# Kernel tuning notes

Measured on AMD Instinct MI355X. Metric: run time of the kernel, lower is better.

Reference implementation:

```python
import jax, jax.numpy as jnp
import numpy as np

B, T, C, H = 4, 2048, 1024, 16
D = C // H


def setup_inputs() -> dict:
    key = jax.random.key(0)
    ks = jax.random.split(key, 6)
    s = 1.0 / np.sqrt(C)
    return {
        "x": jax.random.normal(ks[0], (B, T, C), dtype=jnp.float32),
        "attention_mask": jnp.ones((B, 1, T), dtype=jnp.int32),
        "Wq": jax.random.normal(ks[1], (C, C), dtype=jnp.float32) * s,
        "bq": jnp.zeros((C,), dtype=jnp.float32),
        "Wk": jax.random.normal(ks[2], (C, C), dtype=jnp.float32) * s,
        "bk": jnp.zeros((C,), dtype=jnp.float32),
        "Wv": jax.random.normal(ks[3], (C, C), dtype=jnp.float32) * s,
        "bv": jnp.zeros((C,), dtype=jnp.float32),
        "Wp": jax.random.normal(ks[4], (C, C), dtype=jnp.float32) * s,
        "bp": jnp.zeros((C,), dtype=jnp.float32),
    }


def reference(x, attention_mask, Wq, bq, Wk, bk, Wv, bv, Wp, bp):
    b, t, c = x.shape
    d = c // H
    # projections (torch Linear: x @ W^T + b)
    q = (x @ Wq.T + bq).reshape(b, t, H, d).transpose(0, 2, 1, 3)  # [B,H,T,D]
    k = (x @ Wk.T + bk).reshape(b, t, H, d).transpose(0, 2, 1, 3)
    v = (x @ Wv.T + bv).reshape(b, t, H, d).transpose(0, 2, 1, 3)
    attn = jnp.einsum("bhqd,bhkd->bhqk", q, k) / jnp.sqrt(jnp.asarray(d, x.dtype))
    mask = attention_mask[:, :, :t]  # [B,1,T] -> broadcast over [B,H,T,T] keys
    attn = jnp.where(mask[:, :, None, :] == 0, jnp.asarray(-jnp.inf, x.dtype), attn)
    attn = jax.nn.softmax(attn, axis=-1)  # dropout p=0 (eval)
    y = jnp.einsum("bhqk,bhkd->bhqd", attn, v)
    y = y.transpose(0, 2, 1, 3).reshape(b, t, c)
    return y @ Wp.T + bp
```

## Files before the change

kernel.cpp:

```cpp
#include <hip/hip_runtime.h>


#define TT 2048
#define CC 1024
#define HH 16
#define DD 64
#define BB 4

typedef unsigned short u16;
typedef unsigned int u32;
typedef __attribute__((ext_vector_type(8))) short bf16x8;
typedef __attribute__((ext_vector_type(4))) float f32x4;
typedef __attribute__((ext_vector_type(4))) u32 u32x4;

#if __has_builtin(__builtin_amdgcn_exp2f)
#define EXP2(x) __builtin_amdgcn_exp2f(x)
#else
#define EXP2(x) __expf((x) * 0.6931471805599453f)
#endif

__device__ __forceinline__ u16 f2bf(float f) {
    u32 u = __builtin_bit_cast(u32, f);
    u += 0x7FFFu + ((u >> 16) & 1u);
    return (u16)(u >> 16);
}
__device__ __forceinline__ u32 pk2(float a, float b) {
    u32 ua = __builtin_bit_cast(u32, a); ua += 0x7FFFu + ((ua >> 16) & 1u);
    u32 ub = __builtin_bit_cast(u32, b); ub += 0x7FFFu + ((ub >> 16) & 1u);
    return __builtin_amdgcn_perm(ub, ua, 0x07060302);
}
__device__ __forceinline__ u32 cvtpk(float lo, float hi) {
    u32 r;
    asm("v_cvt_pk_bf16_f32 %0, %1, %2" : "=v"(r) : "v"(lo), "v"(hi));
    return r;
}

#define GLDS(g, l) __builtin_amdgcn_global_load_lds( \
    (const __attribute__((address_space(1))) void*)(g), \
    (__attribute__((address_space(3))) void*)(l), 16, 0, 0)

__global__ __launch_bounds__(256) void wcvt(const float* __restrict__ s,
                                            u16* __restrict__ d, int n8) {
    const int i = blockIdx.x * 256 + threadIdx.x;
    if (i < n8) {
        const float4 f0 = ((const float4*)s)[2 * i];
        const float4 f1 = ((const float4*)s)[2 * i + 1];
        uint4 w;
        w.x = pk2(f0.x, f0.y); w.y = pk2(f0.z, f0.w);
        w.z = pk2(f1.x, f1.y); w.w = pk2(f1.z, f1.w);
        ((uint4*)d)[i] = w;
    }
}

__global__ __launch_bounds__(256) void wcvtA(const float* __restrict__ x,
                                             const float* __restrict__ Wq,
                                             const float* __restrict__ Wk,
                                             const float* __restrict__ Wv,
                                             u16* __restrict__ xb,
                                             u16* __restrict__ Wq16,
                                             u16* __restrict__ Wk16,
                                             u16* __restrict__ Wv16) {
    const int bid = blockIdx.x;
    const float* s; u16* d; int i;
    if (bid < 4096) {
        s = x; d = xb; i = bid * 256 + threadIdx.x;
    } else {
        const int t = bid - 4096;
        const int which = t >> 9, sub = t & 511;
        s = (which == 0) ? Wq : (which == 1) ? Wk : Wv;
        d = (which == 0) ? Wq16 : (which == 1) ? Wk16 : Wv16;
        i = sub * 256 + threadIdx.x;
    }
    const float4 f0 = ((const float4*)s)[2 * i];
    const float4 f1 = ((const float4*)s)[2 * i + 1];
    uint4 w;
    w.x = pk2(f0.x, f0.y); w.y = pk2(f0.z, f0.w);
    w.z = pk2(f1.x, f1.y); w.w = pk2(f1.z, f1.w);
    ((uint4*)d)[i] = w;
}

template <int BN, int WM, int WN, int MODE>
__global__ __launch_bounds__(512, 4) void gemmT(const u16* __restrict__ Ag,
                                                const u16* __restrict__ Bg,
                                                const float* __restrict__ b0,
                                                const float* __restrict__ b1,
                                                const float* __restrict__ b2,
                                                u16* __restrict__ outQ,
                                                u16* __restrict__ outK,
                                                u16* __restrict__ outV,
                                                float* __restrict__ outF) {
    constexpr int NI = WM / 16, NJ = WN / 16;
    constexpr int WAVES_N = BN / WN;
    constexpr int BUFSZ = (256 + BN) * 32;
    constexpr int SPT = 2 + BN / 128;
    constexpr int NT = CC / 32;

    extern __shared__ u16 lds[];
    const int tid  = threadIdx.x;
    const int wave = tid >> 6, lane = tid & 63;
    const int quad = lane >> 4, l16 = lane & 15;
    const int wr = wave / WAVES_N, wc = wave & (WAVES_N - 1);

    constexpr int NBX = (MODE == 0 ? 3072 : 1024) / BN;
    const int bid0 = blockIdx.y * NBX + blockIdx.x;
    const int chunk = (NBX * 32) >> 3;
    const int bid  = (bid0 & 7) * chunk + (bid0 >> 3);
    const int bn = (bid % NBX) * BN, bm = (bid / NBX) * 256;

    u32 aOff[2]; int aDst[2];
#pragma unroll
    for (int g = 0; g < 2; g++) {
        const int c = g * 512 + tid;
        const int row = c >> 2;
        const int kc = (c & 3) ^ ((row >> 1) & 3);
        aOff[g] = (u32)(bm + row) * CC + kc * 8;
        aDst[g] = c * 8;
    }
    u32 bOff[BN / 128]; int bDst[BN / 128];
#pragma unroll
    for (int g = 0; g < BN / 128; g++) {
        const int c = g * 512 + tid;
        const int row = c >> 2;
        const int kc = (c & 3) ^ ((row >> 1) & 3);
        bOff[g] = (u32)(bn + row) * CC + kc * 8;
        bDst[g] = 8192 + c * 8;
    }

    int aRd[NI], bRd[NJ];
#pragma unroll
    for (int i = 0; i < NI; i++) {
        const int row = wr * WM + i * 16 + l16;
        const int p = quad ^ ((row >> 1) & 3);
        aRd[i] = row * 32 + p * 8;
    }
#pragma unroll
    for (int j = 0; j < NJ; j++) {
        const int row = wc * WN + j * 16 + l16;
        const int p = quad ^ ((row >> 1) & 3);
        bRd[j] = 8192 + row * 32 + p * 8;
    }

    f32x4 acc[NI][NJ] = {};

#define STAGE_T(t)                                                        \
    {                                                                     \
        u16* dst = &lds[((t) % 3) * BUFSZ];                               \
        const int k0 = (t) * 32;                                          \
        _Pragma("unroll")                                                 \
        for (int g = 0; g < 2; g++)                                       \
            GLDS(&Ag[(size_t)aOff[g] + k0], &dst[aDst[g]]);               \
        _Pragma("unroll")                                                 \
        for (int g = 0; g < BN / 128; g++)                                \
            GLDS(&Bg[(size_t)bOff[g] + k0], &dst[bDst[g]]);               \
    }

#define COMPUTE_T(t)                                                      \
    {                                                                     \
        const u16* buf = &lds[((t) % 3) * BUFSZ];                         \
        bf16x8 af[NI], bfr[NJ];                                           \
        _Pragma("unroll")                                                 \
        for (int i = 0; i < NI; i++) af[i] = *(const bf16x8*)&buf[aRd[i]];\
        _Pragma("unroll")                                                 \
        for (int j = 0; j < NJ; j++) bfr[j] = *(const bf16x8*)&buf[bRd[j]];\
        __builtin_amdgcn_s_setprio(1);                                    \
        _Pragma("unroll")                                                 \
        for (int i = 0; i < NI; i++)                                      \
            _Pragma("unroll")                                             \
            for (int j = 0; j < NJ; j++)                                  \
                acc[i][j] = __builtin_amdgcn_mfma_f32_16x16x32_bf16(      \
                    af[i], bfr[j], acc[i][j], 0, 0, 0);                   \
        __builtin_amdgcn_s_setprio(0);                                    \
    }

#define WAIT_MAIN()                                                       \
    if constexpr (SPT == 3) asm volatile("s_waitcnt vmcnt(3)" ::: "memory"); \
    else                    asm volatile("s_waitcnt vmcnt(4)" ::: "memory");

    STAGE_T(0); STAGE_T(1);
    WAIT_MAIN();
    __builtin_amdgcn_sched_barrier(0);
    __builtin_amdgcn_s_barrier();
    __builtin_amdgcn_sched_barrier(0);

#pragma unroll 1
    for (int t = 0; t < NT - 2; t++) {
        STAGE_T(t + 2);
        COMPUTE_T(t);
        WAIT_MAIN();
        __builtin_amdgcn_sched_barrier(0);
        __builtin_amdgcn_s_barrier();
        __builtin_amdgcn_sched_barrier(0);
    }
    COMPUTE_T(NT - 2);
    asm volatile("s_waitcnt vmcnt(0)" ::: "memory");
    __builtin_amdgcn_sched_barrier(0);
    __builtin_amdgcn_s_barrier();
    __builtin_amdgcn_sched_barrier(0);
    COMPUTE_T(NT - 1);

#undef STAGE_T
#undef COMPUTE_T
#undef WAIT_MAIN

    if (MODE == 1) {
#pragma unroll
        for (int j = 0; j < NJ; j++) {
            const int col = bn + wc * WN + j * 16 + l16;
            const float bv = b0[col];
#pragma unroll
            for (int i = 0; i < NI; i++) {
                const int row0 = bm + wr * WM + i * 16 + quad * 4;
#pragma unroll
                for (int r = 0; r < 4; r++)
                    outF[(size_t)(row0 + r) * CC + col] = acc[i][j][r] + bv;
            }
        }
    } else {
        const int mid = bn >> 10;
        const float* bias = (mid == 0) ? b0 : (mid == 1) ? b1 : b2;
#pragma unroll
        for (int j = 0; j < NJ; j++) {
            const int col  = bn + wc * WN + j * 16 + l16;
            const int colL = col & (CC - 1);
            const float bv = bias[colL];
#pragma unroll
            for (int i = 0; i < NI; i++) {
                const int row0 = bm + wr * WM + i * 16 + quad * 4;
                if (mid < 2) {
                    u16* out = mid ? outK : outQ;
#pragma unroll
                    for (int r = 0; r < 4; r++)
                        out[(size_t)(row0 + r) * CC + colL] = f2bf(acc[i][j][r] + bv);
                } else {
                    const int hh = colL >> 6, dch = colL & 63;
                    const int bb = row0 >> 11, t0 = row0 & (TT - 1);
                    const size_t idx = (((size_t)bb * HH + hh) * DD + dch) * TT + t0;
                    uint2 w;
                    w.x = pk2(acc[i][j][0] + bv, acc[i][j][1] + bv);
                    w.y = pk2(acc[i][j][2] + bv, acc[i][j][3] + bv);
                    *(uint2*)&outV[idx] = w;
                }
            }
        }
    }
}

__global__ __launch_bounds__(512) void attn(const u16* __restrict__ Q,
                                            const u16* __restrict__ Kb,
                                            const u16* __restrict__ Vt,
                                            const int* __restrict__ mask,
                                            u16* __restrict__ Y) {
    const int b = blockIdx.z, h = blockIdx.y, qt = blockIdx.x;
    const int tid  = threadIdx.x;
    const int wave = tid >> 6, lane = tid & 63;
    const int quad = lane >> 4, l16 = lane & 15;
    const int qrow0 = qt * 256 + wave * 32;

    __shared__ u16 Ks[2][64 * 64];
    __shared__ u16 Vs[2][64 * 64];
    __shared__ __align__(16) float bias_lds[TT];

    const size_t qb = ((size_t)b * TT + qrow0) * CC + h * DD;

    bf16x8 qf[2][2];
#pragma unroll
    for (int m = 0; m < 2; m++)
#pragma unroll
        for (int ks = 0; ks < 2; ks++)
            qf[m][ks] = *(const bf16x8*)&Q[qb + (size_t)(m * 16 + l16) * CC + ks * 32 + quad * 8];

    {
        const int i = tid * 4;
        const int4 m0 = *(const int4*)&mask[b * TT + i];
        bias_lds[i + 0] = m0.x ? 0.f : -1e38f;
        bias_lds[i + 1] = m0.y ? 0.f : -1e38f;
        bias_lds[i + 2] = m0.z ? 0.f : -1e38f;
        bias_lds[i + 3] = m0.w ? 0.f : -1e38f;
    }

    const int c0 = tid;
    const int r0 = c0 >> 3;
    const int kp0 = (c0 & 7) ^ ((((r0 >> 3) & 1) << 2) | (r0 & 3));
    const int vp0 = (c0 & 7) ^ (r0 & 7);
    const u16* kgp = Kb + ((size_t)b * TT) * CC + h * DD;
    const u16* vgp = Vt + ((size_t)(b * HH + h) * DD) * TT;

    const int rowA = ((l16 >> 2) << 3) | (l16 & 3);
    const int s0k  = (((l16 >> 2) & 1) << 2) | (l16 & 3);

    f32x4 o[2][4] = {};
    float lsum[2] = {};
    const float SC = 0.18033688011112042f;

    GLDS(&kgp[(size_t)r0 * CC + kp0 * 8], &Ks[0][c0 * 8]);
    GLDS(&vgp[(size_t)r0 * TT + vp0 * 8], &Vs[0][c0 * 8]);
    asm volatile("s_waitcnt vmcnt(0) lgkmcnt(0)" ::: "memory");
    __builtin_amdgcn_s_barrier();
    __builtin_amdgcn_sched_barrier(0);

#pragma unroll 1
    for (int kt = 0; kt < TT; kt += 64) {
        const int cur = (kt >> 6) & 1;
        const u16* Kc = &Ks[cur][0];
        const u16* Vc = &Vs[cur][0];

        if (kt + 64 < TT) {
            const int nxt = cur ^ 1;
            GLDS(&kgp[(size_t)(kt + 64 + r0) * CC + kp0 * 8], &Ks[nxt][c0 * 8]);
            GLDS(&vgp[(size_t)r0 * TT + kt + 64 + vp0 * 8], &Vs[nxt][c0 * 8]);
        }

        const f32x4 bA = *(const f32x4*)&bias_lds[kt + quad * 8];
        const f32x4 bB = *(const f32x4*)&bias_lds[kt + quad * 8 + 4];
        const f32x4 bC = *(const f32x4*)&bias_lds[kt + 32 + quad * 8];
        const f32x4 bD = *(const f32x4*)&bias_lds[kt + 32 + quad * 8 + 4];

        f32x4 s2[2][4] = {};
        __builtin_amdgcn_s_setprio(1);
#pragma unroll
        for (int n = 0; n < 4; n++) {
            const int rowK = rowA + (n & 1) * 4 + (n >> 1) * 32;
#pragma unroll
            for (int ks = 0; ks < 2; ks++) {
                const int pos = ((ks << 2) + quad) ^ s0k;
                const bf16x8 kf = *(const bf16x8*)&Kc[rowK * 64 + pos * 8];
#pragma unroll
                for (int m = 0; m < 2; m++)
                    s2[m][n] = __builtin_amdgcn_mfma_f32_16x16x32_bf16(kf, qf[m][ks], s2[m][n], 0, 0, 0);
            }
        }
        __builtin_amdgcn_s_setprio(0);

#pragma unroll
        for (int ks = 0; ks < 2; ks++) {
            bf16x8 pf[2];
#pragma unroll
            for (int m = 0; m < 2; m++) {
                u32 pw[4];
#pragma unroll
                for (int nn = 0; nn < 2; nn++) {
                    const int n = 2 * ks + nn;
                    const f32x4 bv = (n == 0) ? bA : (n == 1) ? bB : (n == 2) ? bC : bD;
                    const float p0 = EXP2(fmaf(s2[m][n][0], SC, bv[0]));
                    const float p1 = EXP2(fmaf(s2[m][n][1], SC, bv[1]));
                    const float p2 = EXP2(fmaf(s2[m][n][2], SC, bv[2]));
                    const float p3 = EXP2(fmaf(s2[m][n][3], SC, bv[3]));
                    lsum[m] += (p0 + p1) + (p2 + p3);
                    pw[2 * nn]     = cvtpk(p0, p1);
                    pw[2 * nn + 1] = cvtpk(p2, p3);
                }
                const u32x4 t = { pw[0], pw[1], pw[2], pw[3] };
                pf[m] = __builtin_bit_cast(bf16x8, t);
            }
            __builtin_amdgcn_s_setprio(1);
#pragma unroll
            for (int dt = 0; dt < 4; dt++) {
                const int vrow = dt * 16 + l16;
                const int pos = ((ks << 2) + quad) ^ (vrow & 7);
                const bf16x8 vf = *(const bf16x8*)&Vc[vrow * 64 + pos * 8];
#pragma unroll
                for (int m = 0; m < 2; m++)
                    o[m][dt] = __builtin_amdgcn_mfma_f32_16x16x32_bf16(pf[m], vf, o[m][dt], 0, 0, 0);
            }
            __builtin_amdgcn_s_setprio(0);
        }

        asm volatile("s_waitcnt vmcnt(0)" ::: "memory");
        __builtin_amdgcn_sched_barrier(0);
        __builtin_amdgcn_s_barrier();
    }

#pragma unroll
    for (int m = 0; m < 2; m++) {
        lsum[m] += __shfl_xor(lsum[m], 16, 64);
        lsum[m] += __shfl_xor(lsum[m], 32, 64);
    }

#pragma unroll
    for (int m = 0; m < 2; m++) {
        float inv[4];
#pragma unroll
        for (int r = 0; r < 4; r++)
            inv[r] = 1.0f / __shfl(lsum[m], quad * 4 + r, 64);
#pragma unroll
        for (int dt = 0; dt < 4; dt++)
#pragma unroll
            for (int r = 0; r < 4; r++)
                Y[qb + (size_t)(m * 16 + quad * 4 + r) * CC + dt * 16 + l16] = f2bf(o[m][dt][r] * inv[r]);
    }
}

extern "C" void kernel_launch(void* const* d_in, const int* in_sizes, int n_in,
                              void* d_out, int out_size, void* d_ws, size_t ws_size,
                              hipStream_t stream) {
    const float* x    = (const float*)d_in[0];
    const int*   mask = (const int*)d_in[1];
    const float* Wq   = (const float*)d_in[2];
    const float* bq   = (const float*)d_in[3];
    const float* Wk   = (const float*)d_in[4];
    const float* bk   = (const float*)d_in[5];
    const float* Wv   = (const float*)d_in[6];
    const float* bv   = (const float*)d_in[7];
    const float* Wp   = (const float*)d_in[8];
    const float* bp   = (const float*)d_in[9];

    u16* ws = (u16*)d_ws;
    const size_t sz = (size_t)BB * TT * CC;
    u16* Qb   = ws;
    u16* Kbuf = ws + sz;
    u16* Vtb  = ws + 2 * sz;

    u16* xb   = (u16*)d_out;
    u16* Wq16 = xb + sz;
    u16* Wk16 = Wq16 + (size_t)CC * CC;
    u16* Wv16 = Wk16 + (size_t)CC * CC;

    static bool inited = false;
    if (!inited) {
        (void)hipFuncSetAttribute((const void*)gemmT<128, 64, 64, 0>,
                                  hipFuncAttributeMaxDynamicSharedMemorySize, 73728);
        (void)hipFuncSetAttribute((const void*)gemmT<128, 64, 64, 1>,
                                  hipFuncAttributeMaxDynamicSharedMemorySize, 73728);
        inited = true;
    }

    const int W8 = CC * CC / 8;

    wcvtA<<<5632, 256, 0, stream>>>(x, Wq, Wk, Wv, xb, Wq16, Wk16, Wv16);

    gemmT<128, 64, 64, 0><<<dim3(24, 32), 512, 73728, stream>>>(
        xb, Wq16, bq, bk, bv, Qb, Kbuf, Vtb, nullptr);

    attn<<<dim3(TT / 256, HH, BB), 512, 0, stream>>>(Qb, Kbuf, Vtb, mask, Qb);

    wcvt<<<512, 256, 0, stream>>>(Wp, Kbuf, W8);

    gemmT<128, 64, 64, 1><<<dim3(8, 32), 512, 73728, stream>>>(
        Qb, Kbuf, bp, nullptr, nullptr, nullptr, nullptr, nullptr, (float*)d_out);
}
```

Baseline: 266.4 us.

## Replace QKV projection GEMM with 256x256-tile ping-pong pipelined kernel

Adds a dedicated QKV projection kernel that computes a 256x256 output tile per 512-thread block with BK=64, double-buffered LDS (128 KB), and four sub-phases per k-step. Each sub-phase interleaves partial global-to-LDS prefetch with MFMA compute, separated by barriers. Larger tiles raise arithmetic intensity and cut global traffic, and the phase split aims to overlap loads with compute. The cost is one block per CU, only 384 blocks in total, and heavy register and LDS pressure. The old templated GEMM is trimmed to serve only the output projection.

```diff
diff --git a/kernel.cpp b/kernel.cpp
--- a/kernel.cpp
+++ b/kernel.cpp
@@ -38,6 +38,10 @@
 #define GLDS(g, l) __builtin_amdgcn_global_load_lds( \
     (const __attribute__((address_space(1))) void*)(g), \
     (__attribute__((address_space(3))) void*)(l), 16, 0, 0)
+
+#define PH_SYNC() { __builtin_amdgcn_sched_barrier(0); \
+                    __builtin_amdgcn_s_barrier(); \
+                    __builtin_amdgcn_sched_barrier(0); }
 
 __global__ __launch_bounds__(256) void wcvt(const float* __restrict__ s,
                                             u16* __restrict__ d, int n8) {
@@ -79,15 +83,179 @@
     ((uint4*)d)[i] = w;
 }
 
+__global__ __launch_bounds__(512) void gemm8p(const u16* __restrict__ Ag,
+                                              const u16* __restrict__ Wb,
+                                              const float* __restrict__ b0,
+                                              const float* __restrict__ b1,
+                                              const float* __restrict__ b2,
+                                              u16* __restrict__ outQ,
+                                              u16* __restrict__ outK,
+                                              u16* __restrict__ outV) {
+    extern __shared__ u16 lds[];
+    const int tid  = threadIdx.x;
+    const int wave = tid >> 6, lane = tid & 63;
+    const int quad = lane >> 4, l16 = lane & 15;
+    const int wr = wave >> 2, wc = wave & 3;
+    constexpr int NT = CC / 64;
+
+    const int bid0 = blockIdx.y * 12 + blockIdx.x;
+    const int bid  = (bid0 & 7) * 48 + (bid0 >> 3);
+    const int bn = (bid % 12) * 256, bm = (bid / 12) * 256;
+
+    u32 aOff[4], bOff[4]; int dstOff[4];
+#pragma unroll
+    for (int g = 0; g < 4; g++) {
+        const int c = g * 512 + tid;
+        const int row = c >> 3;
+        const int kc = (c & 7) ^ (row & 7);
+        aOff[g] = (u32)(bm + row) * CC + kc * 8;
+        bOff[g] = (u32)(bn + row) * CC + kc * 8;
+        dstOff[g] = c * 8;
+    }
+
+    int aO[8], bO[4];
+#pragma unroll
+    for (int i = 0; i < 8; i++) {
+        const int row = wr * 128 + i * 16 + l16;
+        aO[i] = row * 64 + (quad ^ (row & 7)) * 8;
+    }
+#pragma unroll
+    for (int j = 0; j < 4; j++) {
+        const int row = wc * 64 + j * 16 + l16;
+        bO[j] = row * 64 + (quad ^ (row & 7)) * 8;
+    }
+
+    f32x4 acc[8][4] = {};
+
+    {
+        u16* An = lds;
+        u16* Bn = lds + 32768;
+        GLDS(&Ag[(size_t)aOff[0]], &An[dstOff[0]]);
+        GLDS(&Ag[(size_t)aOff[2]], &An[dstOff[2]]);
+#pragma unroll
+        for (int g = 0; g < 4; g++) GLDS(&Wb[(size_t)bOff[g]], &Bn[dstOff[g]]);
+        GLDS(&Ag[(size_t)aOff[1]], &An[dstOff[1]]);
+        GLDS(&Ag[(size_t)aOff[3]], &An[dstOff[3]]);
+        asm volatile("s_waitcnt vmcnt(2)" ::: "memory");
+        PH_SYNC();
+    }
+
+#pragma unroll 1
+    for (int t = 0; t < NT; t++) {
+        const u16* Ab = lds + (t & 1) * 16384;
+        const u16* Bb = lds + 32768 + (t & 1) * 16384;
+        u16* An = lds + ((t & 1) ^ 1) * 16384;
+        u16* Bn = lds + 32768 + ((t & 1) ^ 1) * 16384;
+        const int k1 = (t + 1) * 64;
+        const bool pf = (t + 1 < NT);
+
+        bf16x8 af[4], bfr[4];
+
+#pragma unroll
+        for (int j = 0; j < 4; j++) bfr[j] = *(const bf16x8*)&Bb[bO[j]];
+#pragma unroll
+        for (int i = 0; i < 4; i++) af[i] = *(const bf16x8*)&Ab[aO[i]];
+        asm volatile("s_waitcnt lgkmcnt(0)" ::: "memory");
+        __builtin_amdgcn_sched_barrier(0);
+        __builtin_amdgcn_s_setprio(1);
+#pragma unroll
+        for (int i = 0; i < 4; i++)
+#pragma unroll
+            for (int j = 0; j < 4; j++)
+                acc[i][j] = __builtin_amdgcn_mfma_f32_16x16x32_bf16(af[i], bfr[j], acc[i][j], 0, 0, 0);
+        __builtin_amdgcn_s_setprio(0);
+        asm volatile("s_waitcnt vmcnt(0)" ::: "memory");
+        PH_SYNC();
+
+        if (pf) {
+            GLDS(&Ag[(size_t)aOff[0] + k1], &An[dstOff[0]]);
+            GLDS(&Ag[(size_t)aOff[2] + k1], &An[dstOff[2]]);
+        }
+#pragma unroll
+        for (int i = 0; i < 4; i++) af[i] = *(const bf16x8*)&Ab[aO[4 + i]];
+        asm volatile("s_waitcnt lgkmcnt(0)" ::: "memory");
+        __builtin_amdgcn_sched_barrier(0);
+        __builtin_amdgcn_s_setprio(1);
+#pragma unroll
+        for (int i = 0; i < 4; i++)
+#pragma unroll
+            for (int j = 0; j < 4; j++)
+                acc[4 + i][j] = __builtin_amdgcn_mfma_f32_16x16x32_bf16(af[i], bfr[j], acc[4 + i][j], 0, 0, 0);
+        __builtin_amdgcn_s_setprio(0);
+        PH_SYNC();
+
+        if (pf) {
+#pragma unroll
+            for (int g = 0; g < 4; g++)
+                GLDS(&Wb[(size_t)bOff[g] + k1], &Bn[dstOff[g]]);
+        }
+#pragma unroll
+        for (int j = 0; j < 4; j++) bfr[j] = *(const bf16x8*)&Bb[bO[j] ^ 32];
+#pragma unroll
+        for (int i = 0; i < 4; i++) af[i] = *(const bf16x8*)&Ab[aO[i] ^ 32];
+        asm volatile("s_waitcnt lgkmcnt(0)" ::: "memory");
+        __builtin_amdgcn_sched_barrier(0);
+        __builtin_amdgcn_s_setprio(1);
+#pragma unroll
+        for (int i = 0; i < 4; i++)
+#pragma unroll
+            for (int j = 0; j < 4; j++)
+                acc[i][j] = __builtin_amdgcn_mfma_f32_16x16x32_bf16(af[i], bfr[j], acc[i][j], 0, 0, 0);
+        __builtin_amdgcn_s_setprio(0);
+        PH_SYNC();
+
+        if (pf) {
+            GLDS(&Ag[(size_t)aOff[1] + k1], &An[dstOff[1]]);
+            GLDS(&Ag[(size_t)aOff[3] + k1], &An[dstOff[3]]);
+        }
+#pragma unroll
+        for (int i = 0; i < 4; i++) af[i] = *(const bf16x8*)&Ab[aO[4 + i] ^ 32];
+        asm volatile("s_waitcnt lgkmcnt(0)" ::: "memory");
+        __builtin_amdgcn_sched_barrier(0);
+        __builtin_amdgcn_s_setprio(1);
+#pragma unroll
+        for (int i = 0; i < 4; i++)
+#pragma unroll
+            for (int j = 0; j < 4; j++)
+                acc[4 + i][j] = __builtin_amdgcn_mfma_f32_16x16x32_bf16(af[i], bfr[j], acc[4 + i][j], 0, 0, 0);
+        __builtin_amdgcn_s_setprio(0);
+        if (pf) asm volatile("s_waitcnt vmcnt(2)" ::: "memory");
+        else    asm volatile("s_waitcnt vmcnt(0)" ::: "memory");
+        PH_SYNC();
+    }
+
+    const int mid = bn >> 10;
+    const float* bias = (mid == 0) ? b0 : (mid == 1) ? b1 : b2;
+#pragma unroll
+    for (int j = 0; j < 4; j++) {
+        const int col  = bn + wc * 64 + j * 16 + l16;
+        const int colL = col & (CC - 1);
+        const float bv = bias[colL];
+#pragma unroll
+        for (int i = 0; i < 8; i++) {
+            const int row0 = bm + wr * 128 + i * 16 + quad * 4;
+            if (mid < 2) {
+                u16* out = mid ? outK : outQ;
+#pragma unroll
+                for (int r = 0; r < 4; r++)
+                    out[(size_t)(row0 + r) * CC + colL] = f2bf(acc[i][j][r] + bv);
+            } else {
+                const int hh = colL >> 6, dch = colL & 63;
+                const int bb = row0 >> 11, t0 = row0 & (TT - 1);
+                const size_t idx = (((size_t)bb * HH + hh) * DD + dch) * TT + t0;
+                uint2 w;
+                w.x = pk2(acc[i][j][0] + bv, acc[i][j][1] + bv);
+                w.y = pk2(acc[i][j][2] + bv, acc[i][j][3] + bv);
+                *(uint2*)&outV[idx] = w;
+            }
+        }
+    }
+}
+
 template <int BN, int WM, int WN, int MODE>
 __global__ __launch_bounds__(512, 4) void gemmT(const u16* __restrict__ Ag,
                                                 const u16* __restrict__ Bg,
                                                 const float* __restrict__ b0,
-                                                const float* __restrict__ b1,
-                                                const float* __restrict__ b2,
-                                                u16* __restrict__ outQ,
-                                                u16* __restrict__ outK,
-                                                u16* __restrict__ outV,
                                                 float* __restrict__ outF) {
     constexpr int NI = WM / 16, NJ = WN / 16;
     constexpr int WAVES_N = BN / WN;
@@ -101,7 +269,7 @@
     const int quad = lane >> 4, l16 = lane & 15;
     const int wr = wave / WAVES_N, wc = wave & (WAVES_N - 1);
 
-    constexpr int NBX = (MODE == 0 ? 3072 : 1024) / BN;
+    constexpr int NBX = 1024 / BN;
     const int bid0 = blockIdx.y * NBX + blockIdx.x;
     const int chunk = (NBX * 32) >> 3;
     const int bid  = (bid0 & 7) * chunk + (bid0 >> 3);
@@ -130,14 +298,12 @@
 #pragma unroll
     for (int i = 0; i < NI; i++) {
         const int row = wr * WM + i * 16 + l16;
-        const int p = quad ^ ((row >> 1) & 3);
-        aRd[i] = row * 32 + p * 8;
+        aRd[i] = row * 32 + (quad ^ ((row >> 1) & 3)) * 8;
     }
 #pragma unroll
     for (int j = 0; j < NJ; j++) {
         const int row = wc * WN + j * 16 + l16;
-        const int p = quad ^ ((row >> 1) & 3);
-        bRd[j] = 8192 + row * 32 + p * 8;
+        bRd[j] = 8192 + row * 32 + (quad ^ ((row >> 1) & 3)) * 8;
     }
 
     f32x4 acc[NI][NJ] = {};
@@ -178,69 +344,34 @@
 
     STAGE_T(0); STAGE_T(1);
     WAIT_MAIN();
-    __builtin_amdgcn_sched_barrier(0);
-    __builtin_amdgcn_s_barrier();
-    __builtin_amdgcn_sched_barrier(0);
+    PH_SYNC();
 
 #pragma unroll 1
     for (int t = 0; t < NT - 2; t++) {
         STAGE_T(t + 2);
         COMPUTE_T(t);
         WAIT_MAIN();
-        __builtin_amdgcn_sched_barrier(0);
-        __builtin_amdgcn_s_barrier();
-        __builtin_amdgcn_sched_barrier(0);
+        PH_SYNC();
     }
     COMPUTE_T(NT - 2);
     asm volatile("s_waitcnt vmcnt(0)" ::: "memory");
-    __builtin_amdgcn_sched_barrier(0);
-    __builtin_amdgcn_s_barrier();
-    __builtin_amdgcn_sched_barrier(0);
+    PH_SYNC();
     COMPUTE_T(NT - 1);
 
 #undef STAGE_T
 #undef COMPUTE_T
 #undef WAIT_MAIN
 
-    if (MODE == 1) {
-#pragma unroll
-        for (int j = 0; j < NJ; j++) {
-            const int col = bn + wc * WN + j * 16 + l16;
-            const float bv = b0[col];
-#pragma unroll
-            for (int i = 0; i < NI; i++) {
-                const int row0 = bm + wr * WM + i * 16 + quad * 4;
-#pragma unroll
-                for (int r = 0; r < 4; r++)
-                    outF[(size_t)(row0 + r) * CC + col] = acc[i][j][r] + bv;
-            }
-        }
-    } else {
-        const int mid = bn >> 10;
-        const float* bias = (mid == 0) ? b0 : (mid == 1) ? b1 : b2;
-#pragma unroll
-        for (int j = 0; j < NJ; j++) {
-            const int col  = bn + wc * WN + j * 16 + l16;
-            const int colL = col & (CC - 1);
-            const float bv = bias[colL];
-#pragma unroll
-            for (int i = 0; i < NI; i++) {
-                const int row0 = bm + wr * WM + i * 16 + quad * 4;
-                if (mid < 2) {
-                    u16* out = mid ? outK : outQ;
-#pragma unroll
-                    for (int r = 0; r < 4; r++)
-                        out[(size_t)(row0 + r) * CC + colL] = f2bf(acc[i][j][r] + bv);
-                } else {
-                    const int hh = colL >> 6, dch = colL & 63;
-                    const int bb = row0 >> 11, t0 = row0 & (TT - 1);
-                    const size_t idx = (((size_t)bb * HH + hh) * DD + dch) * TT + t0;
-                    uint2 w;
-                    w.x = pk2(acc[i][j][0] + bv, acc[i][j][1] + bv);
-                    w.y = pk2(acc[i][j][2] + bv, acc[i][j][3] + bv);
-                    *(uint2*)&outV[idx] = w;
-                }
-            }
+#pragma unroll
+    for (int j = 0; j < NJ; j++) {
+        const int col = bn + wc * WN + j * 16 + l16;
+        const float bv = b0[col];
+#pragma unroll
+        for (int i = 0; i < NI; i++) {
+            const int row0 = bm + wr * WM + i * 16 + quad * 4;
+#pragma unroll
+            for (int r = 0; r < 4; r++)
+                outF[(size_t)(row0 + r) * CC + col] = acc[i][j][r] + bv;
         }
     }
 }
@@ -417,8 +548,8 @@
 
     static bool inited = false;
     if (!inited) {
-        (void)hipFuncSetAttribute((const void*)gemmT<128, 64, 64, 0>,
-                                  hipFuncAttributeMaxDynamicSharedMemorySize, 73728);
+        (void)hipFuncSetAttribute((const void*)gemm8p,
+                                  hipFuncAttributeMaxDynamicSharedMemorySize, 131072);
         (void)hipFuncSetAttribute((const void*)gemmT<128, 64, 64, 1>,
                                   hipFuncAttributeMaxDynamicSharedMemorySize, 73728);
         inited = true;
@@ -428,13 +559,13 @@
 
     wcvtA<<<5632, 256, 0, stream>>>(x, Wq, Wk, Wv, xb, Wq16, Wk16, Wv16);
 
-    gemmT<128, 64, 64, 0><<<dim3(24, 32), 512, 73728, stream>>>(
-        xb, Wq16, bq, bk, bv, Qb, Kbuf, Vtb, nullptr);
+    gemm8p<<<dim3(12, 32), 512, 131072, stream>>>(
+        xb, Wq16, bq, bk, bv, Qb, Kbuf, Vtb);
 
     attn<<<dim3(TT / 256, HH, BB), 512, 0, stream>>>(Qb, Kbuf, Vtb, mask, Qb);
 
     wcvt<<<512, 256, 0, stream>>>(Wp, Kbuf, W8);
 
     gemmT<128, 64, 64, 1><<<dim3(8, 32), 512, 73728, stream>>>(
-        Qb, Kbuf, bp, nullptr, nullptr, nullptr, nullptr, nullptr, (float*)d_out);
-}
+        Qb, Kbuf, bp, (float*)d_out);
+}
```

New measurement: 291.1 us. +9.3%, slower.

## Parametrize GEMM M-tile, shrink output-projection tile, double K/V tile in attention

Applied to the files above, without the earlier changes.

The GEMM template gains a BM parameter so the output projection can use 128x128 tiles with 32x64 warp tiles. This launches 512 blocks instead of 256 and uses less LDS, to improve CU fill. The attention kernel now loads and processes 128 keys per iteration as two 64-key sub-tiles, halving the number of barriers and wait points per key sweep. The cost is more LDS in attention, which may reduce occupancy, and lower per-block reuse in the projection GEMM.

```diff
diff --git a/kernel.cpp b/kernel.cpp
--- a/kernel.cpp
+++ b/kernel.cpp
@@ -38,6 +38,10 @@
 #define GLDS(g, l) __builtin_amdgcn_global_load_lds( \
     (const __attribute__((address_space(1))) void*)(g), \
     (__attribute__((address_space(3))) void*)(l), 16, 0, 0)
+
+#define PH_SYNC() { __builtin_amdgcn_sched_barrier(0); \
+                    __builtin_amdgcn_s_barrier(); \
+                    __builtin_amdgcn_sched_barrier(0); }
 
 __global__ __launch_bounds__(256) void wcvt(const float* __restrict__ s,
                                             u16* __restrict__ d, int n8) {
@@ -79,7 +83,7 @@
     ((uint4*)d)[i] = w;
 }
 
-template <int BN, int WM, int WN, int MODE>
+template <int BM, int BN, int WM, int WN, int MODE>
 __global__ __launch_bounds__(512, 4) void gemmT(const u16* __restrict__ Ag,
                                                 const u16* __restrict__ Bg,
                                                 const float* __restrict__ b0,
@@ -91,53 +95,54 @@
                                                 float* __restrict__ outF) {
     constexpr int NI = WM / 16, NJ = WN / 16;
     constexpr int WAVES_N = BN / WN;
-    constexpr int BUFSZ = (256 + BN) * 32;
-    constexpr int SPT = 2 + BN / 128;
+    constexpr int BOFF = BM * 32;
+    constexpr int BUFSZ = (BM + BN) * 32;
+    constexpr int AG = BM / 128, BG = BN / 128;
+    constexpr int SPT = AG + BG;
     constexpr int NT = CC / 32;
+    constexpr int NBX = (MODE == 0 ? 3072 : 1024) / BN;
+    constexpr int NBY = 8192 / BM;
 
     extern __shared__ u16 lds[];
     const int tid  = threadIdx.x;
     const int wave = tid >> 6, lane = tid & 63;
     const int quad = lane >> 4, l16 = lane & 15;
-    const int wr = wave / WAVES_N, wc = wave & (WAVES_N - 1);
-
-    constexpr int NBX = (MODE == 0 ? 3072 : 1024) / BN;
+    const int wr = wave / WAVES_N, wc = wave % WAVES_N;
+
     const int bid0 = blockIdx.y * NBX + blockIdx.x;
-    const int chunk = (NBX * 32) >> 3;
+    const int chunk = (NBX * NBY) >> 3;
     const int bid  = (bid0 & 7) * chunk + (bid0 >> 3);
-    const int bn = (bid % NBX) * BN, bm = (bid / NBX) * 256;
-
-    u32 aOff[2]; int aDst[2];
-#pragma unroll
-    for (int g = 0; g < 2; g++) {
+    const int bn = (bid % NBX) * BN, bm = (bid / NBX) * BM;
+
+    u32 aOff[AG]; int aDst[AG];
+#pragma unroll
+    for (int g = 0; g < AG; g++) {
         const int c = g * 512 + tid;
         const int row = c >> 2;
         const int kc = (c & 3) ^ ((row >> 1) & 3);
         aOff[g] = (u32)(bm + row) * CC + kc * 8;
         aDst[g] = c * 8;
     }
-    u32 bOff[BN / 128]; int bDst[BN / 128];
-#pragma unroll
-    for (int g = 0; g < BN / 128; g++) {
+    u32 bOff[BG]; int bDst[BG];
+#pragma unroll
+    for (int g = 0; g < BG; g++) {
         const int c = g * 512 + tid;
         const int row = c >> 2;
         const int kc = (c & 3) ^ ((row >> 1) & 3);
         bOff[g] = (u32)(bn + row) * CC + kc * 8;
-        bDst[g] = 8192 + c * 8;
+        bDst[g] = BOFF + c * 8;
     }
 
     int aRd[NI], bRd[NJ];
 #pragma unroll
     for (int i = 0; i < NI; i++) {
         const int row = wr * WM + i * 16 + l16;
-        const int p = quad ^ ((row >> 1) & 3);
-        aRd[i] = row * 32 + p * 8;
+        aRd[i] = row * 32 + (quad ^ ((row >> 1) & 3)) * 8;
     }
 #pragma unroll
     for (int j = 0; j < NJ; j++) {
         const int row = wc * WN + j * 16 + l16;
-        const int p = quad ^ ((row >> 1) & 3);
-        bRd[j] = 8192 + row * 32 + p * 8;
+        bRd[j] = BOFF + row * 32 + (quad ^ ((row >> 1) & 3)) * 8;
     }
 
     f32x4 acc[NI][NJ] = {};
@@ -147,10 +152,10 @@
         u16* dst = &lds[((t) % 3) * BUFSZ];                               \
         const int k0 = (t) * 32;                                          \
         _Pragma("unroll")                                                 \
-        for (int g = 0; g < 2; g++)                                       \
+        for (int g = 0; g < AG; g++)                                      \
             GLDS(&Ag[(size_t)aOff[g] + k0], &dst[aDst[g]]);               \
         _Pragma("unroll")                                                 \
-        for (int g = 0; g < BN / 128; g++)                                \
+        for (int g = 0; g < BG; g++)                                      \
             GLDS(&Bg[(size_t)bOff[g] + k0], &dst[bDst[g]]);               \
     }
 
@@ -173,29 +178,24 @@
     }
 
 #define WAIT_MAIN()                                                       \
-    if constexpr (SPT == 3) asm volatile("s_waitcnt vmcnt(3)" ::: "memory"); \
-    else                    asm volatile("s_waitcnt vmcnt(4)" ::: "memory");
+    if constexpr (SPT == 2) asm volatile("s_waitcnt vmcnt(2)" ::: "memory"); \
+    else if constexpr (SPT == 3) asm volatile("s_waitcnt vmcnt(3)" ::: "memory"); \
+    else asm volatile("s_waitcnt vmcnt(4)" ::: "memory");
 
     STAGE_T(0); STAGE_T(1);
     WAIT_MAIN();
-    __builtin_amdgcn_sched_barrier(0);
-    __builtin_amdgcn_s_barrier();
-    __builtin_amdgcn_sched_barrier(0);
+    PH_SYNC();
 
 #pragma unroll 1
     for (int t = 0; t < NT - 2; t++) {
         STAGE_T(t + 2);
         COMPUTE_T(t);
         WAIT_MAIN();
-        __builtin_amdgcn_sched_barrier(0);
-        __builtin_amdgcn_s_barrier();
-        __builtin_amdgcn_sched_barrier(0);
+        PH_SYNC();
     }
     COMPUTE_T(NT - 2);
     asm volatile("s_waitcnt vmcnt(0)" ::: "memory");
-    __builtin_amdgcn_sched_barrier(0);
-    __builtin_amdgcn_s_barrier();
-    __builtin_amdgcn_sched_barrier(0);
+    PH_SYNC();
     COMPUTE_T(NT - 1);
 
 #undef STAGE_T
@@ -256,8 +256,8 @@
     const int quad = lane >> 4, l16 = lane & 15;
     const int qrow0 = qt * 256 + wave * 32;
 
-    __shared__ u16 Ks[2][64 * 64];
-    __shared__ u16 Vs[2][64 * 64];
+    __shared__ u16 Ks[2][2][64 * 64];
+    __shared__ u16 Vs[2][2][64 * 64];
     __shared__ __align__(16) float bias_lds[TT];
 
     const size_t qb = ((size_t)b * TT + qrow0) * CC + h * DD;
@@ -292,77 +292,87 @@
     float lsum[2] = {};
     const float SC = 0.18033688011112042f;
 
-    GLDS(&kgp[(size_t)r0 * CC + kp0 * 8], &Ks[0][c0 * 8]);
-    GLDS(&vgp[(size_t)r0 * TT + vp0 * 8], &Vs[0][c0 * 8]);
+    GLDS(&kgp[(size_t)r0 * CC + kp0 * 8],        &Ks[0][0][c0 * 8]);
+    GLDS(&kgp[(size_t)(64 + r0) * CC + kp0 * 8], &Ks[0][1][c0 * 8]);
+    GLDS(&vgp[(size_t)r0 * TT + vp0 * 8],        &Vs[0][0][c0 * 8]);
+    GLDS(&vgp[(size_t)r0 * TT + 64 + vp0 * 8],   &Vs[0][1][c0 * 8]);
     asm volatile("s_waitcnt vmcnt(0) lgkmcnt(0)" ::: "memory");
     __builtin_amdgcn_s_barrier();
     __builtin_amdgcn_sched_barrier(0);
 
 #pragma unroll 1
-    for (int kt = 0; kt < TT; kt += 64) {
-        const int cur = (kt >> 6) & 1;
-        const u16* Kc = &Ks[cur][0];
-        const u16* Vc = &Vs[cur][0];
-
-        if (kt + 64 < TT) {
+    for (int kt = 0; kt < TT; kt += 128) {
+        const int cur = (kt >> 7) & 1;
+
+        if (kt + 128 < TT) {
             const int nxt = cur ^ 1;
-            GLDS(&kgp[(size_t)(kt + 64 + r0) * CC + kp0 * 8], &Ks[nxt][c0 * 8]);
-            GLDS(&vgp[(size_t)r0 * TT + kt + 64 + vp0 * 8], &Vs[nxt][c0 * 8]);
+            const int kt2 = kt + 128;
+            GLDS(&kgp[(size_t)(kt2 + r0) * CC + kp0 * 8],      &Ks[nxt][0][c0 * 8]);
+            GLDS(&kgp[(size_t)(kt2 + 64 + r0) * CC + kp0 * 8], &Ks[nxt][1][c0 * 8]);
+            GLDS(&vgp[(size_t)r0 * TT + kt2 + vp0 * 8],        &Vs[nxt][0][c0 * 8]);
+            GLDS(&vgp[(size_t)r0 * TT + kt2 + 64 + vp0 * 8],   &Vs[nxt][1][c0 * 8]);
         }
 
-        const f32x4 bA = *(const f32x4*)&bias_lds[kt + quad * 8];
-        const f32x4 bB = *(const f32x4*)&bias_lds[kt + quad * 8 + 4];
-        const f32x4 bC = *(const f32x4*)&bias_lds[kt + 32 + quad * 8];
-        const f32x4 bD = *(const f32x4*)&bias_lds[kt + 32 + quad * 8 + 4];
-
-        f32x4 s2[2][4] = {};
-        __builtin_amdgcn_s_setprio(1);
-#pragma unroll
-        for (int n = 0; n < 4; n++) {
-            const int rowK = rowA + (n & 1) * 4 + (n >> 1) * 32;
-#pragma unroll
-            for (int ks = 0; ks < 2; ks++) {
-                const int pos = ((ks << 2) + quad) ^ s0k;
-                const bf16x8 kf = *(const bf16x8*)&Kc[rowK * 64 + pos * 8];
-#pragma unroll
-                for (int m = 0; m < 2; m++)
-                    s2[m][n] = __builtin_amdgcn_mfma_f32_16x16x32_bf16(kf, qf[m][ks], s2[m][n], 0, 0, 0);
-            }
-        }
-        __builtin_amdgcn_s_setprio(0);
-
-#pragma unroll
-        for (int ks = 0; ks < 2; ks++) {
-            bf16x8 pf[2];
-#pragma unroll
-            for (int m = 0; m < 2; m++) {
-                u32 pw[4];
-#pragma unroll
-                for (int nn = 0; nn < 2; nn++) {
-                    const int n = 2 * ks + nn;
-                    const f32x4 bv = (n == 0) ? bA : (n == 1) ? bB : (n == 2) ? bC : bD;
-                    const float p0 = EXP2(fmaf(s2[m][n][0], SC, bv[0]));
-                    const float p1 = EXP2(fmaf(s2[m][n][1], SC, bv[1]));
-                    const float p2 = EXP2(fmaf(s2[m][n][2], SC, bv[2]));
-                    const float p3 = EXP2(fmaf(s2[m][n][3], SC, bv[3]));
-                    lsum[m] += (p0 + p1) + (p2 + p3);
-                    pw[2 * nn]     = cvtpk(p0, p1);
-                    pw[2 * nn + 1] = cvtpk(p2, p3);
+#pragma unroll
+        for (int sx = 0; sx < 2; sx++) {
+            const u16* Kc = &Ks[cur][sx][0];
+            const u16* Vc = &Vs[cur][sx][0];
+            const int kb = kt + sx * 64;
+
+            const f32x4 bA = *(const f32x4*)&bias_lds[kb + quad * 8];
+            const f32x4 bB = *(const f32x4*)&bias_lds[kb + quad * 8 + 4];
+            const f32x4 bC = *(const f32x4*)&bias_lds[kb + 32 + quad * 8];
+            const f32x4 bD = *(const f32x4*)&bias_lds[kb + 32 + quad * 8 + 4];
+
+            f32x4 s2[2][4] = {};
+            __builtin_amdgcn_s_setprio(1);
+#pragma unroll
+            for (int n = 0; n < 4; n++) {
+                const int rowK = rowA + (n & 1) * 4 + (n >> 1) * 32;
+#pragma unroll
+                for (int ks = 0; ks < 2; ks++) {
+                    const int pos = ((ks << 2) + quad) ^ s0k;
+                    const bf16x8 kf = *(const bf16x8*)&Kc[rowK * 64 + pos * 8];
+#pragma unroll
+                    for (int m = 0; m < 2; m++)
+                        s2[m][n] = __builtin_amdgcn_mfma_f32_16x16x32_bf16(kf, qf[m][ks], s2[m][n], 0, 0, 0);
                 }
-                const u32x4 t = { pw[0], pw[1], pw[2], pw[3] };
-                pf[m] = __builtin_bit_cast(bf16x8, t);
-            }
-            __builtin_amdgcn_s_setprio(1);
-#pragma unroll
-            for (int dt = 0; dt < 4; dt++) {
-                const int vrow = dt * 16 + l16;
-                const int pos = ((ks << 2) + quad) ^ (vrow & 7);
-                const bf16x8 vf = *(const bf16x8*)&Vc[vrow * 64 + pos * 8];
-#pragma unroll
-                for (int m = 0; m < 2; m++)
-                    o[m][dt] = __builtin_amdgcn_mfma_f32_16x16x32_bf16(pf[m], vf, o[m][dt], 0, 0, 0);
             }
             __builtin_amdgcn_s_setprio(0);
+
+#pragma unroll
+            for (int ks = 0; ks < 2; ks++) {
+                bf16x8 pf[2];
+#pragma unroll
+                for (int m = 0; m < 2; m++) {
+                    u32 pw[4];
+#pragma unroll
+                    for (int nn = 0; nn < 2; nn++) {
+                        const int n = 2 * ks + nn;
+                        const f32x4 bv = (n == 0) ? bA : (n == 1) ? bB : (n == 2) ? bC : bD;
+                        const float p0 = EXP2(fmaf(s2[m][n][0], SC, bv[0]));
+                        const float p1 = EXP2(fmaf(s2[m][n][1], SC, bv[1]));
+                        const float p2 = EXP2(fmaf(s2[m][n][2], SC, bv[2]));
+                        const float p3 = EXP2(fmaf(s2[m][n][3], SC, bv[3]));
+                        lsum[m] += (p0 + p1) + (p2 + p3);
+                        pw[2 * nn]     = cvtpk(p0, p1);
+                        pw[2 * nn + 1] = cvtpk(p2, p3);
+                    }
+                    const u32x4 t = { pw[0], pw[1], pw[2], pw[3] };
+                    pf[m] = __builtin_bit_cast(bf16x8, t);
+                }
+                __builtin_amdgcn_s_setprio(1);
+#pragma unroll
+                for (int dt = 0; dt < 4; dt++) {
+                    const int vrow = dt * 16 + l16;
+                    const int pos = ((ks << 2) + quad) ^ (vrow & 7);
+                    const bf16x8 vf = *(const bf16x8*)&Vc[vrow * 64 + pos * 8];
+#pragma unroll
+                    for (int m = 0; m < 2; m++)
+                        o[m][dt] = __builtin_amdgcn_mfma_f32_16x16x32_bf16(pf[m], vf, o[m][dt], 0, 0, 0);
+                }
+                __builtin_amdgcn_s_setprio(0);
+            }
         }
 
         asm volatile("s_waitcnt vmcnt(0)" ::: "memory");
@@ -417,10 +427,10 @@
 
     static bool inited = false;
     if (!inited) {
-        (void)hipFuncSetAttribute((const void*)gemmT<128, 64, 64, 0>,
+        (void)hipFuncSetAttribute((const void*)gemmT<256, 128, 64, 64, 0>,
                                   hipFuncAttributeMaxDynamicSharedMemorySize, 73728);
-        (void)hipFuncSetAttribute((const void*)gemmT<128, 64, 64, 1>,
-                                  hipFuncAttributeMaxDynamicSharedMemorySize, 73728);
+        (void)hipFuncSetAttribute((const void*)gemmT<128, 128, 32, 64, 1>,
+                                  hipFuncAttributeMaxDynamicSharedMemorySize, 49152);
         inited = true;
     }
 
@@ -428,13 +438,13 @@
 
     wcvtA<<<5632, 256, 0, stream>>>(x, Wq, Wk, Wv, xb, Wq16, Wk16, Wv16);
 
-    gemmT<128, 64, 64, 0><<<dim3(24, 32), 512, 73728, stream>>>(
+    gemmT<256, 128, 64, 64, 0><<<dim3(24, 32), 512, 73728, stream>>>(
         xb, Wq16, bq, bk, bv, Qb, Kbuf, Vtb, nullptr);
 
     attn<<<dim3(TT / 256, HH, BB), 512, 0, stream>>>(Qb, Kbuf, Vtb, mask, Qb);
 
     wcvt<<<512, 256, 0, stream>>>(Wp, Kbuf, W8);
 
-    gemmT<128, 64, 64, 1><<<dim3(8, 32), 512, 73728, stream>>>(
+    gemmT<128, 128, 32, 64, 1><<<dim3(8, 64), 512, 49152, stream>>>(
         Qb, Kbuf, bp, nullptr, nullptr, nullptr, nullptr, nullptr, (float*)d_out);
 }
```

Measured after the change: 278.0 us. 1.04x slower.
